# Performance work log

Hardware: AMD Instinct MI355X
Metric: run time of the kernel (lower is better)

## Reference

```python
import jax, jax.numpy as jnp
import numpy as np

INDIM = 256
NUM_CENTERS = 1024
OUTDIM = 128
N = 65536


def setup_inputs() -> dict:
    key = jax.random.key(0)
    kx, kc, kw, kb = jax.random.split(key, 4)
    x = jax.random.normal(kx, (N, INDIM), dtype=jnp.float32)
    # centers ~ U(-1, 1), sigmas = 0.1 as in init_centers_sigmas
    centers = jax.random.uniform(kc, (NUM_CENTERS, INDIM), dtype=jnp.float32, minval=-1.0, maxval=1.0)
    sigmas = jnp.full((NUM_CENTERS,), 0.1, dtype=jnp.float32)
    # nn.Linear(num_centers, outdim): weight [outdim, num_centers], bias [outdim]
    bound = 1.0 / np.sqrt(NUM_CENTERS)
    W = jax.random.uniform(kw, (OUTDIM, NUM_CENTERS), dtype=jnp.float32, minval=-bound, maxval=bound)
    b = jax.random.uniform(kb, (OUTDIM,), dtype=jnp.float32, minval=-bound, maxval=bound)
    return {"x": x, "centers": centers, "sigmas": sigmas, "W": W, "b": b}


def reference(x, centers, sigmas, W, b):
    # phi[n, m] = exp(-sigma_m * ||x_n - c_m||^2)
    x_sq = jnp.sum(x * x, axis=1)               # [N]
    c_sq = jnp.sum(centers * centers, axis=1)   # [M]
    cross = jnp.einsum('nd,md->nm', x, centers) # [N, M]
    sqdist = x_sq[:, None] + c_sq[None, :] - 2.0 * cross
    phi = jnp.exp(-sigmas[None, :] * sqdist)    # [N, M]
    return phi @ W.T + b                        # [N, outdim]
```

## Files before the change

### kernel.cpp

```cpp
#include <hip/hip_runtime.h>

typedef __attribute__((ext_vector_type(8))) short bf16x8;
typedef __attribute__((ext_vector_type(4))) float f32x4;
typedef __attribute__((ext_vector_type(2))) long long2v;
typedef unsigned int u32;
typedef unsigned long long u64;

#define LOG2E 1.44269504088896f

__device__ __forceinline__ short f2bf(float f) {
    union { float f; unsigned u; } v; v.f = f;
    unsigned r = v.u + 0x7fffu + ((v.u >> 16) & 1u);
    return (short)(r >> 16);
}

__device__ __forceinline__ u32 f2e4m3(float f) {
    u32 u = __float_as_uint(f);
    u32 sgn = (u >> 24) & 0x80u;
    u32 mag = u & 0x7fffffffu;
    if (mag >= 0x43E00000u) return sgn | 0x7Eu;
    if (mag < 0x3C800000u) {
        u32 q = (u32)(__uint_as_float(mag) * 512.0f + 0.5f);
        return sgn | q;
    }
    u32 r = mag + 0x0007FFFFu + ((mag >> 20) & 1u);
    u32 e8 = ((r >> 23) - 120u) & 0xFu;
    u32 m3 = (r >> 20) & 7u;
    return sgn | (e8 << 3) | m3;
}

__device__ __forceinline__ long pack8_e4m3(float4 a, float4 b) {
    u32 lo = f2e4m3(a.x) | (f2e4m3(a.y) << 8) | (f2e4m3(a.z) << 16) | (f2e4m3(a.w) << 24);
    u32 hi = f2e4m3(b.x) | (f2e4m3(b.y) << 8) | (f2e4m3(b.z) << 16) | (f2e4m3(b.w) << 24);
    return (long)(((u64)hi << 32) | lo);
}

#if __has_builtin(__builtin_amdgcn_exp2f)
#define EXP2(x) __builtin_amdgcn_exp2f(x)
#else
#define EXP2(x) __builtin_exp2f(x)
#endif

__device__ __forceinline__ u32 pack_bf16_trunc(float lo, float hi) {
#if __has_builtin(__builtin_amdgcn_perm)
    return __builtin_amdgcn_perm(__float_as_uint(hi), __float_as_uint(lo), 0x07060302u);
#else
    return (__float_as_uint(hi) & 0xFFFF0000u) | (__float_as_uint(lo) >> 16);
#endif
}

__device__ __forceinline__ void gload16(const void* g, void* l) {
    __builtin_amdgcn_global_load_lds(
        (const __attribute__((address_space(1))) void*)g,
        (__attribute__((address_space(3))) void*)l, 16, 0, 0);
}

__global__ __launch_bounds__(256) void rbf_prep(
    const float* __restrict__ centers, const float* __restrict__ sigmas,
    const float* __restrict__ W,
    char* __restrict__ cfrag8, short* __restrict__ wfrag,
    float* __restrict__ nscsp, float* __restrict__ tsp)
{
    const int tid = threadIdx.x;
    const int bid = blockIdx.x;
    if (bid < 256) {
        const int lane = tid & 63, w = tid >> 6;
        const int m = bid * 4 + w;
        const float4 v = ((const float4*)(centers + (size_t)m * 256))[lane];
        float s = v.x*v.x + v.y*v.y + v.z*v.z + v.w*v.w;
        #pragma unroll
        for (int off = 32; off >= 1; off >>= 1) s += __shfl_xor(s, off, 64);
        if (lane == 0) {
            const float sg = sigmas[m];
            const int c = m >> 5, w5 = m & 31;
            const int g = w5 >> 3, r = w5 & 7, h = r >> 2, j = r & 3;
            const int slot = ((c * 2 + h) * 4 + g) * 4 + j;
            nscsp[slot] = -sg * s * LOG2E;
            tsp[slot]   = 2.0f * sg * LOG2E;
        }
    } else if (bid < 320) {
        const int s = (bid - 256) * 256 + tid;
        const int c = s >> 9, ks = (s >> 6) & 7, lane = s & 63;
        const int l15 = lane & 15;
        const int k = ks * 32 + (lane >> 4) * 8;
        long2v t;
        #pragma unroll
        for (int h = 0; h < 2; ++h) {
            const int m = c * 32 + 8 * (l15 >> 2) + 4 * h + (l15 & 3);
            const float4 a = *(const float4*)(centers + (size_t)m * 256 + k);
            const float4 b = *(const float4*)(centers + (size_t)m * 256 + k + 4);
            t[h] = pack8_e4m3(a, b);
        }
        *(long2v*)(cfrag8 + (size_t)s * 16) = t;
    } else {
        const int s = (bid - 320) * 256 + tid;
        const int c = s >> 9, ot = (s >> 6) & 7, lane = s & 63;
        const int o = ot * 16 + (lane & 15);
        const int k = c * 32 + (lane >> 4) * 8;
        const float4 a = *(const float4*)(W + (size_t)o * 1024 + k);
        const float4 b = *(const float4*)(W + (size_t)o * 1024 + k + 4);
        bf16x8 t;
        t[0]=f2bf(a.x); t[1]=f2bf(a.y); t[2]=f2bf(a.z); t[3]=f2bf(a.w);
        t[4]=f2bf(b.x); t[5]=f2bf(b.y); t[6]=f2bf(b.z); t[7]=f2bf(b.w);
        ((bf16x8*)wfrag)[s] = t;
    }
}

__global__ __launch_bounds__(256, 2) void rbf_main(
    const float* __restrict__ x, const float* __restrict__ bvec,
    const char* __restrict__ cfrag8, const short* __restrict__ wfrag,
    const float* __restrict__ nscsp, const float* __restrict__ tsp,
    float* __restrict__ out)
{
    __shared__ char   Cb8[4][8192];
    __shared__ float4 Tls[512];

    const int tid = threadIdx.x;
    const int lane = tid & 63;
    const int l15 = lane & 15;
    const int g4 = lane >> 4;
    const int w = tid >> 6;
    const int qb = blockIdx.x * 128 + w * 32;

#define STAGE(ci, slot) do {                                                       \
        const char* _cs = cfrag8 + (size_t)(ci) * 8192 + w * 2048 + lane * 16;     \
        gload16(_cs,        &Cb8[(slot)][w * 2048]);                               \
        gload16(_cs + 1024, &Cb8[(slot)][w * 2048 + 1024]);                        \
    } while (0)

#define PREF(ci, rv) do {                                                          \
        const char* _cb = &Cb8[(ci) & 3][0] + (size_t)lane * 16;                   \
        _Pragma("unroll")                                                          \
        for (int ks = 0; ks < 8; ++ks) rv[ks] = *(const long2v*)(_cb + ks * 1024); \
    } while (0)

#define SEXPR(rv, cc, pa0, pa1) do {                                               \
        f32x4 s00 = (f32x4){0.f,0.f,0.f,0.f}, s01 = s00, s10 = s00, s11 = s00;     \
        _Pragma("unroll")                                                          \
        for (int ks = 0; ks < 8; ++ks) {                                           \
            s00 = __builtin_amdgcn_mfma_f32_16x16x32_fp8_fp8(rv[ks][0], xq8[0][ks], s00, 0, 0, 0); \
            s10 = __builtin_amdgcn_mfma_f32_16x16x32_fp8_fp8(rv[ks][0], xq8[1][ks], s10, 0, 0, 0); \
            s01 = __builtin_amdgcn_mfma_f32_16x16x32_fp8_fp8(rv[ks][1], xq8[0][ks], s01, 0, 0, 0); \
            s11 = __builtin_amdgcn_mfma_f32_16x16x32_fp8_fp8(rv[ks][1], xq8[1][ks], s11, 0, 0, 0); \
        }                                                                          \
        const int base0 = ((cc) * 2 + 0) * 4 + g4;                                 \
        const int base1 = ((cc) * 2 + 1) * 4 + g4;                                 \
        const float4 q0 = Tls[base0];                                              \
        const float4 t0 = Tls[256 + base0];                                        \
        const float4 q1 = Tls[base1];                                              \
        const float4 t1 = Tls[256 + base1];                                        \
        const float* q0p = (const float*)&q0; const float* t0p = (const float*)&t0;\
        const float* q1p = (const float*)&q1; const float* t1p = (const float*)&t1;\
        float p00[4], p01[4], p10[4], p11[4];                                      \
        _Pragma("unroll")                                                          \
        for (int j = 0; j < 4; ++j) {                                              \
            p00[j] = EXP2(fmaf(t0p[j], s00[j] - hxs0, q0p[j]));                    \
            p01[j] = EXP2(fmaf(t1p[j], s01[j] - hxs0, q1p[j]));                    \
            p10[j] = EXP2(fmaf(t0p[j], s10[j] - hxs1, q0p[j]));                    \
            p11[j] = EXP2(fmaf(t1p[j], s11[j] - hxs1, q1p[j]));                    \
        }                                                                          \
        pa0.u[0] = pack_bf16_trunc(p00[0], p00[1]);                                \
        pa0.u[1] = pack_bf16_trunc(p00[2], p00[3]);                                \
        pa0.u[2] = pack_bf16_trunc(p01[0], p01[1]);                                \
        pa0.u[3] = pack_bf16_trunc(p01[2], p01[3]);                                \
        pa1.u[0] = pack_bf16_trunc(p10[0], p10[1]);                                \
        pa1.u[1] = pack_bf16_trunc(p10[2], p10[3]);                                \
        pa1.u[2] = pack_bf16_trunc(p11[0], p11[1]);                                \
        pa1.u[3] = pack_bf16_trunc(p11[2], p11[3]);                                \
    } while (0)

#define PVX(pa0, pa1, wv) do {                                                     \
        _Pragma("unroll")                                                          \
        for (int ot = 0; ot < 8; ++ot) {                                           \
            acc[0][ot] = __builtin_amdgcn_mfma_f32_16x16x32_bf16(pa0.v, wv[ot], acc[0][ot], 0, 0, 0); \
            acc[1][ot] = __builtin_amdgcn_mfma_f32_16x16x32_bf16(pa1.v, wv[ot], acc[1][ot], 0, 0, 0); \
        }                                                                          \
    } while (0)

#define CHUNK(c, cur, nxt) do {                                                    \
        bf16x8 wv[8];                                                              \
        _Pragma("unroll")                                                          \
        for (int f = 0; f < 8; ++f) wv[f] = wsrc[(size_t)(c) * 512 + f * 64];      \
        if ((c) <= 28) STAGE((c) + 3, ((c) + 3) & 3);                              \
        if ((c) <= 30) PREF((c) + 1, nxt);                                         \
        union { u32 u[4]; bf16x8 v; } pa0, pa1;                                    \
        SEXPR(cur, (c), pa0, pa1);                                                 \
        PVX(pa0, pa1, wv);                                                         \
        if ((c) < 31) {                                                            \
            if ((c) <= 28) { asm volatile("s_waitcnt vmcnt(2)" ::: "memory"); }    \
            else           { asm volatile("s_waitcnt vmcnt(0)" ::: "memory"); }    \
            __builtin_amdgcn_s_barrier();                                          \
        }                                                                          \
    } while (0)

    STAGE(0, 0);
    STAGE(1, 1);
    STAGE(2, 2);

    Tls[tid]       = ((const float4*)nscsp)[tid];
    Tls[256 + tid] = ((const float4*)tsp)[tid];

    long xq8[2][8];
    float xs[2];
    #pragma unroll
    for (int t = 0; t < 2; ++t) {
        const float* xr = x + (size_t)(qb + t * 16 + l15) * 256 + g4 * 8;
        float ss = 0.f;
        #pragma unroll
        for (int ks = 0; ks < 8; ++ks) {
            const float4 a = *(const float4*)(xr + ks * 32);
            const float4 b = *(const float4*)(xr + ks * 32 + 4);
            ss += a.x*a.x + a.y*a.y + a.z*a.z + a.w*a.w
                + b.x*b.x + b.y*b.y + b.z*b.z + b.w*b.w;
            xq8[t][ks] = pack8_e4m3(a, b);
        }
        ss += __shfl_xor(ss, 16, 64);
        ss += __shfl_xor(ss, 32, 64);
        xs[t] = ss;
    }
    const float hxs0 = 0.5f * xs[0];
    const float hxs1 = 0.5f * xs[1];

    f32x4 acc[2][8];
    #pragma unroll
    for (int t = 0; t < 2; ++t)
        #pragma unroll
        for (int ot = 0; ot < 8; ++ot) acc[t][ot] = (f32x4){0.f, 0.f, 0.f, 0.f};

    __syncthreads();

    const bf16x8* wsrc = (const bf16x8*)wfrag + lane;

    long2v rX[8], rY[8];
    PREF(0, rX);

    #pragma unroll 2
    for (int i = 0; i < 16; ++i) {
        CHUNK(2 * i,     rX, rY);
        CHUNK(2 * i + 1, rY, rX);
    }

    #pragma unroll
    for (int t = 0; t < 2; ++t) {
        #pragma unroll
        for (int jr = 0; jr < 4; ++jr) {
            const int q = qb + t * 16 + g4 * 4 + jr;
            #pragma unroll
            for (int ot = 0; ot < 8; ++ot)
                out[(size_t)q * 128 + ot * 16 + l15] = acc[t][ot][jr] + bvec[ot * 16 + l15];
        }
    }
#undef STAGE
#undef PREF
#undef SEXPR
#undef PVX
#undef CHUNK
}

extern "C" void kernel_launch(void* const* d_in, const int* in_sizes, int n_in,
                              void* d_out, int out_size, void* d_ws, size_t ws_size,
                              hipStream_t stream) {
    (void)in_sizes; (void)n_in; (void)out_size; (void)ws_size;
    const float* x       = (const float*)d_in[0];
    const float* centers = (const float*)d_in[1];
    const float* sigmas  = (const float*)d_in[2];
    const float* W       = (const float*)d_in[3];
    const float* b       = (const float*)d_in[4];
    float* out = (float*)d_out;

    char*  cfrag8 = (char*)d_ws;
    short* wfrag  = (short*)(cfrag8 + 16384 * 16);
    float* nscsp  = (float*)(wfrag + 16384 * 8);
    float* tsp    = nscsp + 1024;

    rbf_prep<<<384, 256, 0, stream>>>(centers, sigmas, W, cfrag8, wfrag, nscsp, tsp);
    rbf_main<<<512, 256, 0, stream>>>(x, b, cfrag8, wfrag, nscsp, tsp, out);
}
```

Baseline: 70.51 us.

## Switch cross-product GEMM to 16x16x128 scaled FP8 MFMA with relaid fragments

Replaces the 16x16x32 FP8 MFMAs with the gfx950 16x16x128 f8f6f4 scaled MFMA (unit scales), so each chunk needs 8 instructions instead of 32. Center fragments and x registers are re-laid out so each lane holds 32 contiguous K bytes. The register double-buffered LDS prefetch (PREF) and the two-chunk manual unroll are removed, and LDS reads now happen inside the compute step. The aim is fewer, higher-throughput MFMA issues, at the cost of losing the prefetch overlap and exposing LDS latency.

```diff
diff --git a/kernel.cpp b/kernel.cpp
--- a/kernel.cpp
+++ b/kernel.cpp
@@ -3,6 +3,7 @@
 typedef __attribute__((ext_vector_type(8))) short bf16x8;
 typedef __attribute__((ext_vector_type(4))) float f32x4;
 typedef __attribute__((ext_vector_type(2))) long long2v;
+typedef __attribute__((ext_vector_type(8))) int i32x8;
 typedef unsigned int u32;
 typedef unsigned long long u64;
 
@@ -54,6 +55,18 @@
         (const __attribute__((address_space(1))) void*)g,
         (__attribute__((address_space(3))) void*)l, 16, 0, 0);
 }
+
+#if __has_builtin(__builtin_amdgcn_mfma_scale_f32_16x16x128_f8f6f4)
+#define MFMA128(A, B, C) \
+    C = __builtin_amdgcn_mfma_scale_f32_16x16x128_f8f6f4((A), (B), (C), 0, 0, 0, 0x7F7F7F7F, 0, 0x7F7F7F7F)
+#else
+#define MFMA128(A, B, C) do {                                                      \
+        union { i32x8 v; long l[4]; } _a, _b; _a.v = (A); _b.v = (B);              \
+        _Pragma("unroll")                                                          \
+        for (int _dp = 0; _dp < 4; ++_dp)                                          \
+            C = __builtin_amdgcn_mfma_f32_16x16x32_fp8_fp8(_a.l[_dp], _b.l[_dp], (C), 0, 0, 0); \
+    } while (0)
+#endif
 
 __global__ __launch_bounds__(256) void rbf_prep(
     const float* __restrict__ centers, const float* __restrict__ sigmas,
@@ -80,17 +93,19 @@
         }
     } else if (bid < 320) {
         const int s = (bid - 256) * 256 + tid;
-        const int c = s >> 9, ks = (s >> 6) & 7, lane = s & 63;
-        const int l15 = lane & 15;
-        const int k = ks * 32 + (lane >> 4) * 8;
+        const int c = s >> 9, h2k = (s >> 7) & 3, piece = (s >> 6) & 1, lane = s & 63;
+        const int h = h2k >> 1, ks = h2k & 1;
+        const int l15 = lane & 15, g4 = lane >> 4;
+        const int m = c * 32 + 8 * (l15 >> 2) + 4 * h + (l15 & 3);
+        const int kb = ks * 128 + g4 * 32 + piece * 16;
+        const float* cp = centers + (size_t)m * 256 + kb;
+        const float4 a0 = *(const float4*)(cp);
+        const float4 a1 = *(const float4*)(cp + 4);
+        const float4 a2 = *(const float4*)(cp + 8);
+        const float4 a3 = *(const float4*)(cp + 12);
         long2v t;
-        #pragma unroll
-        for (int h = 0; h < 2; ++h) {
-            const int m = c * 32 + 8 * (l15 >> 2) + 4 * h + (l15 & 3);
-            const float4 a = *(const float4*)(centers + (size_t)m * 256 + k);
-            const float4 b = *(const float4*)(centers + (size_t)m * 256 + k + 4);
-            t[h] = pack8_e4m3(a, b);
-        }
+        t[0] = pack8_e4m3(a0, a1);
+        t[1] = pack8_e4m3(a2, a3);
         *(long2v*)(cfrag8 + (size_t)s * 16) = t;
     } else {
         const int s = (bid - 320) * 256 + tid;
@@ -128,21 +143,20 @@
         gload16(_cs + 1024, &Cb8[(slot)][w * 2048 + 1024]);                        \
     } while (0)
 
-#define PREF(ci, rv) do {                                                          \
-        const char* _cb = &Cb8[(ci) & 3][0] + (size_t)lane * 16;                   \
-        _Pragma("unroll")                                                          \
-        for (int ks = 0; ks < 8; ++ks) rv[ks] = *(const long2v*)(_cb + ks * 1024); \
-    } while (0)
-
-#define SEXPR(rv, cc, pa0, pa1) do {                                               \
-        f32x4 s00 = (f32x4){0.f,0.f,0.f,0.f}, s01 = s00, s10 = s00, s11 = s00;     \
-        _Pragma("unroll")                                                          \
-        for (int ks = 0; ks < 8; ++ks) {                                           \
-            s00 = __builtin_amdgcn_mfma_f32_16x16x32_fp8_fp8(rv[ks][0], xq8[0][ks], s00, 0, 0, 0); \
-            s10 = __builtin_amdgcn_mfma_f32_16x16x32_fp8_fp8(rv[ks][0], xq8[1][ks], s10, 0, 0, 0); \
-            s01 = __builtin_amdgcn_mfma_f32_16x16x32_fp8_fp8(rv[ks][1], xq8[0][ks], s01, 0, 0, 0); \
-            s11 = __builtin_amdgcn_mfma_f32_16x16x32_fp8_fp8(rv[ks][1], xq8[1][ks], s11, 0, 0, 0); \
-        }                                                                          \
+#define Z4 (f32x4){0.f,0.f,0.f,0.f}
+
+#define SEXPR(slot, cc, pa0, pa1) do {                                             \
+        const char* cb = &Cb8[(slot)][0] + (size_t)lane * 16;                      \
+        union { long2v p[2]; i32x8 v; } A0, A1, A2, A3;                            \
+        A0.p[0] = *(const long2v*)(cb);          A0.p[1] = *(const long2v*)(cb + 1024); \
+        A1.p[0] = *(const long2v*)(cb + 2048);   A1.p[1] = *(const long2v*)(cb + 3072); \
+        A2.p[0] = *(const long2v*)(cb + 4096);   A2.p[1] = *(const long2v*)(cb + 5120); \
+        A3.p[0] = *(const long2v*)(cb + 6144);   A3.p[1] = *(const long2v*)(cb + 7168); \
+        f32x4 s00 = Z4, s01 = Z4, s10 = Z4, s11 = Z4;                              \
+        MFMA128(A0.v, xq00, s00);  MFMA128(A0.v, xq10, s10);                       \
+        MFMA128(A1.v, xq01, s00);  MFMA128(A1.v, xq11, s10);                       \
+        MFMA128(A2.v, xq00, s01);  MFMA128(A2.v, xq10, s11);                       \
+        MFMA128(A3.v, xq01, s01);  MFMA128(A3.v, xq11, s11);                       \
         const int base0 = ((cc) * 2 + 0) * 4 + g4;                                 \
         const int base1 = ((cc) * 2 + 1) * 4 + g4;                                 \
         const float4 q0 = Tls[base0];                                              \
@@ -177,22 +191,6 @@
         }                                                                          \
     } while (0)
 
-#define CHUNK(c, cur, nxt) do {                                                    \
-        bf16x8 wv[8];                                                              \
-        _Pragma("unroll")                                                          \
-        for (int f = 0; f < 8; ++f) wv[f] = wsrc[(size_t)(c) * 512 + f * 64];      \
-        if ((c) <= 28) STAGE((c) + 3, ((c) + 3) & 3);                              \
-        if ((c) <= 30) PREF((c) + 1, nxt);                                         \
-        union { u32 u[4]; bf16x8 v; } pa0, pa1;                                    \
-        SEXPR(cur, (c), pa0, pa1);                                                 \
-        PVX(pa0, pa1, wv);                                                         \
-        if ((c) < 31) {                                                            \
-            if ((c) <= 28) { asm volatile("s_waitcnt vmcnt(2)" ::: "memory"); }    \
-            else           { asm volatile("s_waitcnt vmcnt(0)" ::: "memory"); }    \
-            __builtin_amdgcn_s_barrier();                                          \
-        }                                                                          \
-    } while (0)
-
     STAGE(0, 0);
     STAGE(1, 1);
     STAGE(2, 2);
@@ -200,19 +198,26 @@
     Tls[tid]       = ((const float4*)nscsp)[tid];
     Tls[256 + tid] = ((const float4*)tsp)[tid];
 
-    long xq8[2][8];
+    i32x8 xq00, xq01, xq10, xq11;
     float xs[2];
     #pragma unroll
     for (int t = 0; t < 2; ++t) {
-        const float* xr = x + (size_t)(qb + t * 16 + l15) * 256 + g4 * 8;
+        const float* xr = x + (size_t)(qb + t * 16 + l15) * 256;
         float ss = 0.f;
         #pragma unroll
-        for (int ks = 0; ks < 8; ++ks) {
-            const float4 a = *(const float4*)(xr + ks * 32);
-            const float4 b = *(const float4*)(xr + ks * 32 + 4);
-            ss += a.x*a.x + a.y*a.y + a.z*a.z + a.w*a.w
-                + b.x*b.x + b.y*b.y + b.z*b.z + b.w*b.w;
-            xq8[t][ks] = pack8_e4m3(a, b);
+        for (int ks = 0; ks < 2; ++ks) {
+            union { long lg[4]; i32x8 v; } xx;
+            const float* xb = xr + ks * 128 + g4 * 32;
+            #pragma unroll
+            for (int q8 = 0; q8 < 4; ++q8) {
+                const float4 a = *(const float4*)(xb + q8 * 8);
+                const float4 b = *(const float4*)(xb + q8 * 8 + 4);
+                ss += a.x*a.x + a.y*a.y + a.z*a.z + a.w*a.w
+                    + b.x*b.x + b.y*b.y + b.z*b.z + b.w*b.w;
+                xx.lg[q8] = pack8_e4m3(a, b);
+            }
+            if (t == 0) { if (ks == 0) xq00 = xx.v; else xq01 = xx.v; }
+            else        { if (ks == 0) xq10 = xx.v; else xq11 = xx.v; }
         }
         ss += __shfl_xor(ss, 16, 64);
         ss += __shfl_xor(ss, 32, 64);
@@ -225,19 +230,30 @@
     #pragma unroll
     for (int t = 0; t < 2; ++t)
         #pragma unroll
-        for (int ot = 0; ot < 8; ++ot) acc[t][ot] = (f32x4){0.f, 0.f, 0.f, 0.f};
+        for (int ot = 0; ot < 8; ++ot) acc[t][ot] = Z4;
 
     __syncthreads();
 
     const bf16x8* wsrc = (const bf16x8*)wfrag + lane;
 
-    long2v rX[8], rY[8];
-    PREF(0, rX);
-
-    #pragma unroll 2
-    for (int i = 0; i < 16; ++i) {
-        CHUNK(2 * i,     rX, rY);
-        CHUNK(2 * i + 1, rY, rX);
+    for (int c = 0; c < 32; ++c) {
+        const int slot = c & 3;
+
+        bf16x8 wv[8];
+        #pragma unroll
+        for (int f = 0; f < 8; ++f) wv[f] = wsrc[(size_t)c * 512 + f * 64];
+
+        if (c <= 28) STAGE(c + 3, (c + 3) & 3);
+
+        union { u32 u[4]; bf16x8 v; } pa0, pa1;
+        SEXPR(slot, c, pa0, pa1);
+        PVX(pa0, pa1, wv);
+
+        if (c < 31) {
+            if (c <= 28) { asm volatile("s_waitcnt vmcnt(2)" ::: "memory"); }
+            else         { asm volatile("s_waitcnt vmcnt(0)" ::: "memory"); }
+            __builtin_amdgcn_s_barrier();
+        }
     }
 
     #pragma unroll
@@ -251,10 +267,9 @@
         }
     }
 #undef STAGE
-#undef PREF
 #undef SEXPR
 #undef PVX
-#undef CHUNK
+#undef Z4
 }
 
 extern "C" void kernel_launch(void* const* d_in, const int* in_sizes, int n_in,
```

Result: faster. 68.24 us (-3.2%).
